# Kernel optimization log

Hardware: AMD Instinct MI355X
Metric: run time of the kernel (lower is better)

The kernel has to match this reference:

```python
import jax, jax.numpy as jnp
import numpy as np

N = 8192
F_IN = 128
F_OUT = 128


def setup_inputs() -> dict:
    key = jax.random.key(0)
    k1, k2, k3, k4, k5 = jax.random.split(key, 5)
    x = jax.random.normal(k1, (N, F_IN), dtype=jnp.float32)
    adj = jax.random.uniform(k2, (N, N), dtype=jnp.float32)
    kernel = jax.random.normal(k3, (F_IN, F_OUT), dtype=jnp.float32) * 0.05
    bias = jax.random.normal(k4, (F_OUT,), dtype=jnp.float32) * 0.05
    beta = jax.random.uniform(k5, (N,), dtype=jnp.float32)
    return {"x": x, "adj": adj, "kernel": kernel, "bias": bias, "beta": beta}


def reference(x, adj, kernel, bias, beta):
    # torch: diag(1/(adj.sum(1)+beta)) @ (adj + diag(beta)) @ x @ kernel + bias
    # (adj + diag(beta)) @ x  ==  adj @ x + beta[:, None] * x  (no NxN temp)
    inv_deg = 1.0 / (jnp.sum(adj, axis=1) + beta)        # [N]
    agg = adj @ x + beta[:, None] * x                     # [N, F_in]
    out = (inv_deg[:, None] * agg) @ kernel + bias        # [N, F_out]
    return out
```

## Files before the change

### kernel.cpp

```cpp
#include <hip/hip_runtime.h>

#define NN 8192
#define FD 128
#define BK 64
#define LDSR 72

typedef float f32x4 __attribute__((ext_vector_type(4)));
typedef short short8 __attribute__((ext_vector_type(8)));
typedef unsigned short ushort4v __attribute__((ext_vector_type(4)));
typedef unsigned short ushort8v __attribute__((ext_vector_type(8)));

__device__ __forceinline__ unsigned short f2bf(float f) {
  unsigned int u = __builtin_bit_cast(unsigned int, f);
  u += 0x7fffu + ((u >> 16) & 1u);
  return (unsigned short)(u >> 16);
}
__device__ __forceinline__ float bf2f(unsigned short h) {
  unsigned int u = ((unsigned int)h) << 16;
  return __builtin_bit_cast(float, u);
}

__global__ __launch_bounds__(256) void xk_kernel(
    const float* __restrict__ x, const float* __restrict__ kern,
    unsigned short* __restrict__ bfrag, unsigned short* __restrict__ xk_rm) {
  __shared__ __align__(16) unsigned short kl[FD * FD];
  __shared__ __align__(16) float xl[16 * FD];
  const int t = threadIdx.x;
  const int row0 = blockIdx.x * 16;

  #pragma unroll
  for (int j = 0; j < 16; ++j) {
    int idx = (j * 256 + t) * 4;
    f32x4 kv = *(const f32x4*)&kern[idx];
    ushort4v kw;
    #pragma unroll
    for (int q = 0; q < 4; ++q) kw[q] = f2bf(kv[q]);
    *(ushort4v*)&kl[idx] = kw;
  }
  #pragma unroll
  for (int j = 0; j < 2; ++j) {
    int idx = (j * 256 + t) * 4;
    *(f32x4*)&xl[idx] = *(const f32x4*)&x[(size_t)row0 * FD + idx];
  }
  __syncthreads();

  const int r0 = (t >> 5) * 2;
  const int c0 = (t & 31) * 4;
  float acc[2][4] = {};
  #pragma unroll 4
  for (int k = 0; k < FD; ++k) {
    ushort4v kq = *(const ushort4v*)&kl[k * FD + c0];
    float kv[4];
    #pragma unroll
    for (int q = 0; q < 4; ++q) kv[q] = bf2f(kq[q]);
    float x0 = xl[r0 * FD + k];
    float x1 = xl[(r0 + 1) * FD + k];
    #pragma unroll
    for (int q = 0; q < 4; ++q) {
      acc[0][q] += x0 * kv[q];
      acc[1][q] += x1 * kv[q];
    }
  }
  #pragma unroll
  for (int i = 0; i < 2; ++i) {
    const int r = row0 + r0 + i;
    const int kt = r >> 5;
    const int lhi = ((r >> 3) & 3) * 16;
    const int j = r & 7;
    ushort4v ow;
    #pragma unroll
    for (int q = 0; q < 4; ++q) {
      const int c = c0 + q;
      unsigned short bv = f2bf(acc[i][q]);
      ow[q] = bv;
      bfrag[(((size_t)kt * 8 + (c >> 4)) * 64 + (lhi + (c & 15))) * 8 + j] = bv;
    }
    *(ushort4v*)&xk_rm[(size_t)r * FD + c0] = ow;
  }
}

#define PREFETCH(Lr, stp)                                                     \
  do {                                                                        \
    _Pragma("unroll") for (int i = 0; i < 8; ++i)                             \
        Lr[i] = *(const f32x4*)(ap + (size_t)i * 4 * NN + (stp) * BK);        \
  } while (0)

#define STAGE(Lr, bufofs)                                                     \
  do {                                                                        \
    _Pragma("unroll") for (int i = 0; i < 8; ++i) {                           \
      ushort4v cw;                                                            \
      _Pragma("unroll") for (int q = 0; q < 4; ++q) cw[q] = f2bf(Lr[i][q]);   \
      rs[i] += Lr[i][0] + Lr[i][1] + Lr[i][2] + Lr[i][3];                     \
      *(ushort4v*)&sw[(bufofs) + wofs + i * 4 * LDSR] = cw;                   \
    }                                                                         \
  } while (0)

#define LOAD_B(stp)                                                           \
  do {                                                                        \
    const int ktg = kt0 + (stp) * 2;                                          \
    _Pragma("unroll") for (int h = 0; h < 2; ++h)                             \
        _Pragma("unroll") for (int cb = 0; cb < 8; ++cb)                      \
            Bf[h][cb] = *(const ushort8v*)(bp +                               \
                (((size_t)(ktg + h) * 8 + cb) << 9));                         \
  } while (0)

#define MFMA_CLUSTER(bufofs)                                                  \
  do {                                                                        \
    __builtin_amdgcn_s_setprio(1);                                            \
    _Pragma("unroll") for (int h = 0; h < 2; ++h) {                           \
      const int abase = (bufofs) + h * 32 + (l >> 4) * 8;                     \
      short8 aF0 = *(const short8*)&sw[abase + (l & 15) * LDSR];              \
      short8 aF1 = *(const short8*)&sw[abase + (16 + (l & 15)) * LDSR];       \
      _Pragma("unroll") for (int cb = 0; cb < 8; ++cb) {                      \
        acc[0][cb] = __builtin_amdgcn_mfma_f32_16x16x32_bf16(                 \
            aF0, Bf[h][cb], acc[0][cb], 0, 0, 0);                             \
        acc[1][cb] = __builtin_amdgcn_mfma_f32_16x16x32_bf16(                 \
            aF1, Bf[h][cb], acc[1][cb], 0, 0, 0);                             \
      }                                                                       \
    }                                                                         \
    __builtin_amdgcn_s_setprio(0);                                            \
  } while (0)

template <int S>
__global__ __launch_bounds__(256, 2) void gcn_mm(
    const float* __restrict__ adj, const unsigned short* __restrict__ bfrag,
    unsigned short* __restrict__ parts, float* __restrict__ rowpart) {
  constexpr int KW = NN / S;
  constexpr int NS = KW / BK;
  __shared__ __align__(16) unsigned short sA[4][2][32 * LDSR];

  const int t = threadIdx.x;
  const int l = t & 63;
  const int w = t >> 6;
  const int b = blockIdx.x;
  const int s = b & (S - 1);
  const int row0 = (b / S) * 128 + w * 32;
  const int kbase = s * KW;
  const int kt0 = s * (KW / 32);

  const float* ap = adj + (size_t)(row0 + (l >> 4)) * NN + kbase + (l & 15) * 4;
  unsigned short* sw = &sA[w][0][0];
  const int wofs = (l >> 4) * LDSR + (l & 15) * 4;
  const int B1OFS = 32 * LDSR;
  const unsigned short* bp = bfrag + (size_t)l * 8;

  f32x4 LrA[8], LrB[8];
  ushort8v Bf[2][8];
  f32x4 acc[2][8] = {};
  float rs[8] = {0.f, 0.f, 0.f, 0.f, 0.f, 0.f, 0.f, 0.f};

  PREFETCH(LrA, 0);
  STAGE(LrA, 0);
  PREFETCH(LrB, 1);

  for (int st = 0; st < NS; st += 2) {
    LOAD_B(st);
    if (st + 2 < NS) PREFETCH(LrA, st + 2);
    __builtin_amdgcn_sched_barrier(0);
    MFMA_CLUSTER(0);
    STAGE(LrB, B1OFS);
    LOAD_B(st + 1);
    if (st + 3 < NS) PREFETCH(LrB, st + 3);
    __builtin_amdgcn_sched_barrier(0);
    MFMA_CLUSTER(B1OFS);
    if (st + 2 < NS) STAGE(LrA, 0);
  }

  #pragma unroll
  for (int i = 0; i < 8; ++i) {
    rs[i] += __shfl_xor(rs[i], 1);
    rs[i] += __shfl_xor(rs[i], 2);
    rs[i] += __shfl_xor(rs[i], 4);
    rs[i] += __shfl_xor(rs[i], 8);
  }
  if ((l & 15) == 0) {
    #pragma unroll
    for (int i = 0; i < 8; ++i)
      rowpart[(size_t)s * NN + row0 + i * 4 + (l >> 4)] = rs[i];
  }

  unsigned short* pp = parts + ((size_t)s * NN + row0) * FD;
  #pragma unroll
  for (int rf = 0; rf < 2; ++rf)
    #pragma unroll
    for (int cb = 0; cb < 8; ++cb)
      #pragma unroll
      for (int j = 0; j < 4; ++j) {
        const int r = rf * 16 + ((l >> 4) << 2) + j;
        pp[(size_t)r * FD + cb * 16 + (l & 15)] = f2bf(acc[rf][cb][j]);
      }
}

__global__ __launch_bounds__(256) void gcn_fin(
    const unsigned short* __restrict__ parts, const float* __restrict__ rowpart,
    const unsigned short* __restrict__ xk_rm, const float* __restrict__ beta,
    const float* __restrict__ bias, float* __restrict__ out, int S) {
  const int t = threadIdx.x;
  const int r = blockIdx.x * 16 + (t >> 4);
  const int c0 = (t & 15) * 8;

  float rsum = 0.f;
  for (int s = 0; s < S; ++s) rsum += rowpart[(size_t)s * NN + r];
  const float bt = beta[r];
  const float inv = 1.0f / (rsum + bt);

  float a[8] = {0.f, 0.f, 0.f, 0.f, 0.f, 0.f, 0.f, 0.f};
  for (int s = 0; s < S; ++s) {
    ushort8v pv = *(const ushort8v*)&parts[((size_t)s * NN + r) * FD + c0];
    #pragma unroll
    for (int q = 0; q < 8; ++q) a[q] += bf2f(pv[q]);
  }
  ushort8v xv = *(const ushort8v*)&xk_rm[(size_t)r * FD + c0];
  f32x4 o0, o1;
  #pragma unroll
  for (int q = 0; q < 4; ++q) {
    o0[q] = (a[q] + bt * bf2f(xv[q])) * inv + bias[c0 + q];
    o1[q] = (a[4 + q] + bt * bf2f(xv[4 + q])) * inv + bias[c0 + 4 + q];
  }
  *(f32x4*)&out[(size_t)r * FD + c0] = o0;
  *(f32x4*)&out[(size_t)r * FD + c0 + 4] = o1;
}

extern "C" void kernel_launch(void* const* d_in, const int* in_sizes, int n_in,
                              void* d_out, int out_size, void* d_ws, size_t ws_size,
                              hipStream_t stream) {
  const float* x    = (const float*)d_in[0];
  const float* adj  = (const float*)d_in[1];
  const float* kern = (const float*)d_in[2];
  const float* bias = (const float*)d_in[3];
  const float* beta = (const float*)d_in[4];
  float* out = (float*)d_out;

  char* ws = (char*)d_ws;
  unsigned short* bfrag = (unsigned short*)ws;
  unsigned short* xk_rm = (unsigned short*)(ws + (size_t)NN * FD * 2);
  const size_t off_rowpart = (size_t)NN * FD * 4;
  float* rowpart = (float*)(ws + off_rowpart);
  const size_t off_parts = off_rowpart + (size_t)8 * NN * 4;
  unsigned short* parts = (unsigned short*)(ws + off_parts);

  int S = 8;
  while (S > 1 && off_parts + (size_t)S * NN * FD * 2 > ws_size) S >>= 1;

  hipLaunchKernelGGL(xk_kernel, dim3(NN / 16), dim3(256), 0, stream,
                     x, kern, bfrag, xk_rm);

  dim3 blk(256);
  switch (S) {
    case 8: hipLaunchKernelGGL(gcn_mm<8>, dim3(64 * 8), blk, 0, stream, adj, bfrag, parts, rowpart); break;
    case 4: hipLaunchKernelGGL(gcn_mm<4>, dim3(64 * 4), blk, 0, stream, adj, bfrag, parts, rowpart); break;
    case 2: hipLaunchKernelGGL(gcn_mm<2>, dim3(64 * 2), blk, 0, stream, adj, bfrag, parts, rowpart); break;
    default: hipLaunchKernelGGL(gcn_mm<1>, dim3(64), blk, 0, stream, adj, bfrag, parts, rowpart); break;
  }

  hipLaunchKernelGGL(gcn_fin, dim3(NN / 16), dim3(256), 0, stream,
                     parts, rowpart, xk_rm, beta, bias, out, S);
}
```

Measured before the change: 84.83 us.

## Widen adj k-tile to 128 with XOR-swizzled LDS and single prefetch buffer

Each stage now covers a 128-wide k slice instead of 64. Each lane loads 16 float4s spanning two rows at a time, so one row is read as a contiguous 512-byte segment. The padded LDS rows are replaced by 128-wide rows with an XOR swizzle to avoid bank conflicts, and the two register prefetch sets are merged into one 16-entry set. The aim is fewer loop iterations and better-coalesced global reads, at the cost of more registers held per in-flight prefetch and a changed overlap schedule.

```diff
diff --git a/kernel.cpp b/kernel.cpp
--- a/kernel.cpp
+++ b/kernel.cpp
@@ -2,8 +2,7 @@
 
 #define NN 8192
 #define FD 128
-#define BK 64
-#define LDSR 72
+#define BKW 128
 
 typedef float f32x4 __attribute__((ext_vector_type(4)));
 typedef short short8 __attribute__((ext_vector_type(8)));
@@ -79,45 +78,52 @@
   }
 }
 
-#define PREFETCH(Lr, stp)                                                     \
-  do {                                                                        \
-    _Pragma("unroll") for (int i = 0; i < 8; ++i)                             \
-        Lr[i] = *(const f32x4*)(ap + (size_t)i * 4 * NN + (stp) * BK);        \
-  } while (0)
-
-#define STAGE(Lr, bufofs)                                                     \
-  do {                                                                        \
-    _Pragma("unroll") for (int i = 0; i < 8; ++i) {                           \
+#define PREF_A(stp)                                                           \
+  do {                                                                        \
+    _Pragma("unroll") for (int i = 0; i < 16; ++i)                            \
+        Lr[i] = *(const f32x4*)(ap + (size_t)2 * i * NN + (stp) * BKW);       \
+  } while (0)
+
+#define STAGE_A(bufofs)                                                       \
+  do {                                                                        \
+    _Pragma("unroll") for (int i = 0; i < 16; ++i) {                          \
       ushort4v cw;                                                            \
       _Pragma("unroll") for (int q = 0; q < 4; ++q) cw[q] = f2bf(Lr[i][q]);   \
       rs[i] += Lr[i][0] + Lr[i][1] + Lr[i][2] + Lr[i][3];                     \
-      *(ushort4v*)&sw[(bufofs) + wofs + i * 4 * LDSR] = cw;                   \
+      const int row_l = 2 * i + rl2;                                          \
+      *(ushort4v*)&sw0[(bufofs) + row_l * 128 +                               \
+                       (kc4 ^ ((row_l & 7) << 3))] = cw;                      \
     }                                                                         \
   } while (0)
 
-#define LOAD_B(stp)                                                           \
-  do {                                                                        \
-    const int ktg = kt0 + (stp) * 2;                                          \
+#define LOAD_B2(ktg)                                                          \
+  do {                                                                        \
     _Pragma("unroll") for (int h = 0; h < 2; ++h)                             \
         _Pragma("unroll") for (int cb = 0; cb < 8; ++cb)                      \
             Bf[h][cb] = *(const ushort8v*)(bp +                               \
-                (((size_t)(ktg + h) * 8 + cb) << 9));                         \
-  } while (0)
-
-#define MFMA_CLUSTER(bufofs)                                                  \
-  do {                                                                        \
+                (((size_t)((ktg) + h) * 8 + cb) << 9));                       \
+  } while (0)
+
+#define CMP2(bufofs, ktl)                                                     \
+  do {                                                                        \
+    short8 aF0[2], aF1[2];                                                    \
+    _Pragma("unroll") for (int h = 0; h < 2; ++h) {                           \
+      const int colu = ((ktl) + h) * 32 + (l >> 4) * 8;                       \
+      const int ra = l & 15;                                                  \
+      const int rb2 = 16 + ra;                                                \
+      aF0[h] = *(const short8*)&sw0[(bufofs) + ra * 128 +                     \
+                                    (colu ^ ((ra & 7) << 3))];                \
+      aF1[h] = *(const short8*)&sw0[(bufofs) + rb2 * 128 +                    \
+                                    (colu ^ ((rb2 & 7) << 3))];               \
+    }                                                                         \
     __builtin_amdgcn_s_setprio(1);                                            \
-    _Pragma("unroll") for (int h = 0; h < 2; ++h) {                           \
-      const int abase = (bufofs) + h * 32 + (l >> 4) * 8;                     \
-      short8 aF0 = *(const short8*)&sw[abase + (l & 15) * LDSR];              \
-      short8 aF1 = *(const short8*)&sw[abase + (16 + (l & 15)) * LDSR];       \
-      _Pragma("unroll") for (int cb = 0; cb < 8; ++cb) {                      \
-        acc[0][cb] = __builtin_amdgcn_mfma_f32_16x16x32_bf16(                 \
-            aF0, Bf[h][cb], acc[0][cb], 0, 0, 0);                             \
-        acc[1][cb] = __builtin_amdgcn_mfma_f32_16x16x32_bf16(                 \
-            aF1, Bf[h][cb], acc[1][cb], 0, 0, 0);                             \
-      }                                                                       \
-    }                                                                         \
+    _Pragma("unroll") for (int h = 0; h < 2; ++h)                             \
+        _Pragma("unroll") for (int cb = 0; cb < 8; ++cb) {                    \
+          acc[0][cb] = __builtin_amdgcn_mfma_f32_16x16x32_bf16(               \
+              aF0[h], Bf[h][cb], acc[0][cb], 0, 0, 0);                        \
+          acc[1][cb] = __builtin_amdgcn_mfma_f32_16x16x32_bf16(               \
+              aF1[h], Bf[h][cb], acc[1][cb], 0, 0, 0);                        \
+        }                                                                     \
     __builtin_amdgcn_s_setprio(0);                                            \
   } while (0)
 
@@ -126,8 +132,9 @@
     const float* __restrict__ adj, const unsigned short* __restrict__ bfrag,
     unsigned short* __restrict__ parts, float* __restrict__ rowpart) {
   constexpr int KW = NN / S;
-  constexpr int NS = KW / BK;
-  __shared__ __align__(16) unsigned short sA[4][2][32 * LDSR];
+  constexpr int NS = KW / BKW;
+  constexpr int BUFO = 32 * 128;
+  __shared__ unsigned short sA[4][2][BUFO];
 
   const int t = threadIdx.x;
   const int l = t & 63;
@@ -138,45 +145,48 @@
   const int kbase = s * KW;
   const int kt0 = s * (KW / 32);
 
-  const float* ap = adj + (size_t)(row0 + (l >> 4)) * NN + kbase + (l & 15) * 4;
-  unsigned short* sw = &sA[w][0][0];
-  const int wofs = (l >> 4) * LDSR + (l & 15) * 4;
-  const int B1OFS = 32 * LDSR;
+  const int rl2 = l >> 5;
+  const int kc4 = (l & 31) * 4;
+  const float* ap = adj + (size_t)(row0 + rl2) * NN + kbase + kc4;
+
+  unsigned short* sw0 = &sA[w][0][0];
   const unsigned short* bp = bfrag + (size_t)l * 8;
 
-  f32x4 LrA[8], LrB[8];
+  f32x4 Lr[16];
   ushort8v Bf[2][8];
   f32x4 acc[2][8] = {};
-  float rs[8] = {0.f, 0.f, 0.f, 0.f, 0.f, 0.f, 0.f, 0.f};
-
-  PREFETCH(LrA, 0);
-  STAGE(LrA, 0);
-  PREFETCH(LrB, 1);
-
-  for (int st = 0; st < NS; st += 2) {
-    LOAD_B(st);
-    if (st + 2 < NS) PREFETCH(LrA, st + 2);
+  float rs[16] = {};
+
+  PREF_A(0);
+  STAGE_A(0);
+
+  for (int st = 0; st < NS; ++st) {
+    const int bo = (st & 1) * BUFO;
+    const int nbo = bo ^ BUFO;
+    const int ktg = kt0 + st * 4;
+    LOAD_B2(ktg);
     __builtin_amdgcn_sched_barrier(0);
-    MFMA_CLUSTER(0);
-    STAGE(LrB, B1OFS);
-    LOAD_B(st + 1);
-    if (st + 3 < NS) PREFETCH(LrB, st + 3);
+    if (st + 1 < NS) PREF_A(st + 1);
     __builtin_amdgcn_sched_barrier(0);
-    MFMA_CLUSTER(B1OFS);
-    if (st + 2 < NS) STAGE(LrA, 0);
-  }
-
-  #pragma unroll
-  for (int i = 0; i < 8; ++i) {
+    CMP2(bo, 0);
+    LOAD_B2(ktg + 2);
+    __builtin_amdgcn_sched_barrier(0);
+    CMP2(bo, 2);
+    if (st + 1 < NS) STAGE_A(nbo);
+  }
+
+  #pragma unroll
+  for (int i = 0; i < 16; ++i) {
     rs[i] += __shfl_xor(rs[i], 1);
     rs[i] += __shfl_xor(rs[i], 2);
     rs[i] += __shfl_xor(rs[i], 4);
     rs[i] += __shfl_xor(rs[i], 8);
-  }
-  if ((l & 15) == 0) {
-    #pragma unroll
-    for (int i = 0; i < 8; ++i)
-      rowpart[(size_t)s * NN + row0 + i * 4 + (l >> 4)] = rs[i];
+    rs[i] += __shfl_xor(rs[i], 16);
+  }
+  if ((l & 31) == 0) {
+    #pragma unroll
+    for (int i = 0; i < 16; ++i)
+      rowpart[(size_t)s * NN + row0 + 2 * i + rl2] = rs[i];
   }
 
   unsigned short* pp = parts + ((size_t)s * NN + row0) * FD;
```

After: 81.14 us. 4.4% less time.

## Share A tile across waves with swizzled LDS and split output columns per wave

Applied to the files above, without the earlier changes.

Restructures the main adjacency GEMM so each block handles 32 rows instead of 128. The four waves now cooperatively stage one 32x128 bf16 A tile into XOR-swizzled shared memory, and each wave computes a distinct 32-column slice of the output instead of all 128 columns. BK doubles to 128, register use per thread drops (fewer accumulators and B fragments), launch bounds allow 4 blocks per CU, and the grid grows fourfold. The cost is block-wide barriers every half-step, plus redundant B fragment loads across blocks with the same k-slice.

```diff
diff --git a/kernel.cpp b/kernel.cpp
--- a/kernel.cpp
+++ b/kernel.cpp
@@ -2,8 +2,7 @@
 
 #define NN 8192
 #define FD 128
-#define BK 64
-#define LDSR 72
+#define BK 128
 
 typedef float f32x4 __attribute__((ext_vector_type(4)));
 typedef short short8 __attribute__((ext_vector_type(8)));
@@ -79,115 +78,129 @@
   }
 }
 
-#define PREFETCH(Lr, stp)                                                     \
-  do {                                                                        \
-    _Pragma("unroll") for (int i = 0; i < 8; ++i)                             \
-        Lr[i] = *(const f32x4*)(ap + (size_t)i * 4 * NN + (stp) * BK);        \
-  } while (0)
-
-#define STAGE(Lr, bufofs)                                                     \
-  do {                                                                        \
-    _Pragma("unroll") for (int i = 0; i < 8; ++i) {                           \
+#define PREF(Lr, stp)                                                         \
+  do {                                                                        \
+    _Pragma("unroll") for (int i = 0; i < 4; ++i)                             \
+        Lr[i] = *(const f32x4*)(ap + (size_t)(i * 8) * NN + (stp) * BK);      \
+  } while (0)
+
+#define STAGE(Lr, buf)                                                        \
+  do {                                                                        \
+    _Pragma("unroll") for (int i = 0; i < 4; ++i) {                           \
       ushort4v cw;                                                            \
       _Pragma("unroll") for (int q = 0; q < 4; ++q) cw[q] = f2bf(Lr[i][q]);   \
       rs[i] += Lr[i][0] + Lr[i][1] + Lr[i][2] + Lr[i][3];                     \
-      *(ushort4v*)&sw[(bufofs) + wofs + i * 4 * LDSR] = cw;                   \
+      const int row_l = i * 8 + srow;                                         \
+      *(ushort4v*)&sA[buf][row_l * 128 +                                      \
+                           (scol ^ ((row_l & 7) << 3))] = cw;                 \
     }                                                                         \
   } while (0)
 
 #define LOAD_B(stp)                                                           \
   do {                                                                        \
-    const int ktg = kt0 + (stp) * 2;                                          \
-    _Pragma("unroll") for (int h = 0; h < 2; ++h)                             \
-        _Pragma("unroll") for (int cb = 0; cb < 8; ++cb)                      \
-            Bf[h][cb] = *(const ushort8v*)(bp +                               \
-                (((size_t)(ktg + h) * 8 + cb) << 9));                         \
-  } while (0)
-
-#define MFMA_CLUSTER(bufofs)                                                  \
+    const int ktg = kt0 + (stp) * 4;                                          \
+    _Pragma("unroll") for (int kk = 0; kk < 4; ++kk)                          \
+        _Pragma("unroll") for (int ci = 0; ci < 2; ++ci)                      \
+            Bf[kk * 2 + ci] = *(const ushort8v*)(bp +                         \
+                (((size_t)(ktg + kk) * 8 + (w * 2 + ci)) << 9));              \
+  } while (0)
+
+#define MFMA_STEP(buf)                                                        \
   do {                                                                        \
     __builtin_amdgcn_s_setprio(1);                                            \
-    _Pragma("unroll") for (int h = 0; h < 2; ++h) {                           \
-      const int abase = (bufofs) + h * 32 + (l >> 4) * 8;                     \
-      short8 aF0 = *(const short8*)&sw[abase + (l & 15) * LDSR];              \
-      short8 aF1 = *(const short8*)&sw[abase + (16 + (l & 15)) * LDSR];       \
-      _Pragma("unroll") for (int cb = 0; cb < 8; ++cb) {                      \
-        acc[0][cb] = __builtin_amdgcn_mfma_f32_16x16x32_bf16(                 \
-            aF0, Bf[h][cb], acc[0][cb], 0, 0, 0);                             \
-        acc[1][cb] = __builtin_amdgcn_mfma_f32_16x16x32_bf16(                 \
-            aF1, Bf[h][cb], acc[1][cb], 0, 0, 0);                             \
+    _Pragma("unroll") for (int kk = 0; kk < 4; ++kk) {                        \
+      short8 aF[2];                                                           \
+      _Pragma("unroll") for (int mf = 0; mf < 2; ++mf) {                      \
+        const int r = mf * 16 + (l & 15);                                     \
+        const int colu = kk * 32 + (l >> 4) * 8;                              \
+        aF[mf] = *(const short8*)&sA[buf][r * 128 +                           \
+                                          (colu ^ ((r & 7) << 3))];           \
       }                                                                       \
+      _Pragma("unroll") for (int mf = 0; mf < 2; ++mf)                        \
+          _Pragma("unroll") for (int ci = 0; ci < 2; ++ci)                    \
+              acc[mf][ci] = __builtin_amdgcn_mfma_f32_16x16x32_bf16(          \
+                  aF[mf], Bf[kk * 2 + ci], acc[mf][ci], 0, 0, 0);             \
     }                                                                         \
     __builtin_amdgcn_s_setprio(0);                                            \
   } while (0)
 
+#define LDS_BARRIER()                                                         \
+  do {                                                                        \
+    asm volatile("s_waitcnt lgkmcnt(0)" ::: "memory");                        \
+    __builtin_amdgcn_sched_barrier(0);                                        \
+    __builtin_amdgcn_s_barrier();                                             \
+  } while (0)
+
 template <int S>
-__global__ __launch_bounds__(256, 2) void gcn_mm(
+__global__ __launch_bounds__(256, 4) void gcn_mm(
     const float* __restrict__ adj, const unsigned short* __restrict__ bfrag,
     unsigned short* __restrict__ parts, float* __restrict__ rowpart) {
   constexpr int KW = NN / S;
   constexpr int NS = KW / BK;
-  __shared__ __align__(16) unsigned short sA[4][2][32 * LDSR];
+  __shared__ unsigned short sA[2][32 * 128];
 
   const int t = threadIdx.x;
   const int l = t & 63;
   const int w = t >> 6;
   const int b = blockIdx.x;
   const int s = b & (S - 1);
-  const int row0 = (b / S) * 128 + w * 32;
+  const int row0 = (b / S) * 32;
   const int kbase = s * KW;
   const int kt0 = s * (KW / 32);
 
-  const float* ap = adj + (size_t)(row0 + (l >> 4)) * NN + kbase + (l & 15) * 4;
-  unsigned short* sw = &sA[w][0][0];
-  const int wofs = (l >> 4) * LDSR + (l & 15) * 4;
-  const int B1OFS = 32 * LDSR;
+  const int srow = t >> 5;
+  const int scol = (t & 31) * 4;
+  const float* ap = adj + (size_t)(row0 + srow) * NN + kbase + scol;
   const unsigned short* bp = bfrag + (size_t)l * 8;
 
-  f32x4 LrA[8], LrB[8];
-  ushort8v Bf[2][8];
-  f32x4 acc[2][8] = {};
-  float rs[8] = {0.f, 0.f, 0.f, 0.f, 0.f, 0.f, 0.f, 0.f};
-
-  PREFETCH(LrA, 0);
+  f32x4 LrA[4], LrB[4];
+  ushort8v Bf[8];
+  f32x4 acc[2][2] = {};
+  float rs[4] = {};
+
+  PREF(LrA, 0);
   STAGE(LrA, 0);
-  PREFETCH(LrB, 1);
+  PREF(LrB, 1);
+  LDS_BARRIER();
 
   for (int st = 0; st < NS; st += 2) {
     LOAD_B(st);
-    if (st + 2 < NS) PREFETCH(LrA, st + 2);
+    if (st + 2 < NS) PREF(LrA, st + 2);
     __builtin_amdgcn_sched_barrier(0);
-    MFMA_CLUSTER(0);
-    STAGE(LrB, B1OFS);
+    MFMA_STEP(0);
+    STAGE(LrB, 1);
+    LDS_BARRIER();
     LOAD_B(st + 1);
-    if (st + 3 < NS) PREFETCH(LrB, st + 3);
+    if (st + 3 < NS) PREF(LrB, st + 3);
     __builtin_amdgcn_sched_barrier(0);
-    MFMA_CLUSTER(B1OFS);
+    MFMA_STEP(1);
     if (st + 2 < NS) STAGE(LrA, 0);
-  }
-
-  #pragma unroll
-  for (int i = 0; i < 8; ++i) {
+    LDS_BARRIER();
+  }
+
+  #pragma unroll
+  for (int i = 0; i < 4; ++i) {
     rs[i] += __shfl_xor(rs[i], 1);
     rs[i] += __shfl_xor(rs[i], 2);
     rs[i] += __shfl_xor(rs[i], 4);
     rs[i] += __shfl_xor(rs[i], 8);
-  }
-  if ((l & 15) == 0) {
-    #pragma unroll
-    for (int i = 0; i < 8; ++i)
-      rowpart[(size_t)s * NN + row0 + i * 4 + (l >> 4)] = rs[i];
-  }
-
-  unsigned short* pp = parts + ((size_t)s * NN + row0) * FD;
-  #pragma unroll
-  for (int rf = 0; rf < 2; ++rf)
-    #pragma unroll
-    for (int cb = 0; cb < 8; ++cb)
+    rs[i] += __shfl_xor(rs[i], 16);
+  }
+  if ((l & 31) == 0) {
+    #pragma unroll
+    for (int i = 0; i < 4; ++i)
+      rowpart[(size_t)s * NN + row0 + i * 8 + srow] = rs[i];
+  }
+
+  unsigned short* pp = parts + ((size_t)s * NN + row0) * FD + w * 32;
+  #pragma unroll
+  for (int mf = 0; mf < 2; ++mf)
+    #pragma unroll
+    for (int ci = 0; ci < 2; ++ci)
       #pragma unroll
       for (int j = 0; j < 4; ++j) {
-        const int r = rf * 16 + ((l >> 4) << 2) + j;
-        pp[(size_t)r * FD + cb * 16 + (l & 15)] = f2bf(acc[rf][cb][j]);
+        const int r = mf * 16 + ((l >> 4) << 2) + j;
+        pp[(size_t)r * FD + ci * 16 + (l & 15)] = f2bf(acc[mf][ci][j]);
       }
 }
 
@@ -247,10 +260,10 @@
 
   dim3 blk(256);
   switch (S) {
-    case 8: hipLaunchKernelGGL(gcn_mm<8>, dim3(64 * 8), blk, 0, stream, adj, bfrag, parts, rowpart); break;
-    case 4: hipLaunchKernelGGL(gcn_mm<4>, dim3(64 * 4), blk, 0, stream, adj, bfrag, parts, rowpart); break;
-    case 2: hipLaunchKernelGGL(gcn_mm<2>, dim3(64 * 2), blk, 0, stream, adj, bfrag, parts, rowpart); break;
-    default: hipLaunchKernelGGL(gcn_mm<1>, dim3(64), blk, 0, stream, adj, bfrag, parts, rowpart); break;
+    case 8: hipLaunchKernelGGL(gcn_mm<8>, dim3(256 * 8), blk, 0, stream, adj, bfrag, parts, rowpart); break;
+    case 4: hipLaunchKernelGGL(gcn_mm<4>, dim3(256 * 4), blk, 0, stream, adj, bfrag, parts, rowpart); break;
+    case 2: hipLaunchKernelGGL(gcn_mm<2>, dim3(256 * 2), blk, 0, stream, adj, bfrag, parts, rowpart); break;
+    default: hipLaunchKernelGGL(gcn_mm<1>, dim3(256), blk, 0, stream, adj, bfrag, parts, rowpart); break;
   }
 
   hipLaunchKernelGGL(gcn_fin, dim3(NN / 16), dim3(256), 0, stream,
```

New measurement: 80.73 us, median of 3. 1.05x faster.
